# Kernel optimization log

Measured on AMD Instinct MI355X. Metric: run time of the kernel, lower is better.

The kernel has to match this reference:

```python
import jax, jax.numpy as jnp
import numpy as np

D_MODEL, D_INNER, D_STATE, HEADDIM, NHEADS, D_CONV, EPS = 2048, 4096, 64, 64, 64, 4, 1e-5
CONV_DIM = D_INNER + 2 * D_STATE  # ngroups=1


def setup_inputs() -> dict:
    key = jax.random.key(0)
    ks = jax.random.split(key, 8)
    return {
        "hidden_states": jax.random.normal(ks[0], (2, 2048, D_MODEL), jnp.float32),
        "rms_weight": jnp.ones((D_MODEL,), jnp.float32),
        "in_proj_w": jax.random.normal(ks[1], (2 * D_INNER + 2 * D_STATE + NHEADS, D_MODEL), jnp.float32) * 0.02,
        "conv_w": jax.random.normal(ks[2], (CONV_DIM, D_CONV), jnp.float32) * 0.2,
        "conv_b": jnp.zeros((CONV_DIM,), jnp.float32),
        "dt_bias": jax.random.normal(ks[3], (NHEADS,), jnp.float32) * 0.5,
        "A_log": jax.random.uniform(ks[4], (NHEADS,), jnp.float32, 0.0, 1.0),
        "D": jnp.ones((NHEADS,), jnp.float32),
        "norm_w": jnp.ones((D_INNER,), jnp.float32),
        "out_proj_w": jax.random.normal(ks[5], (D_MODEL, D_INNER), jnp.float32) * 0.02,
    }


def _rmsnorm(x, w, eps=EPS):
    var = jnp.mean(jnp.square(x), axis=-1, keepdims=True)
    return x * jax.lax.rsqrt(var + eps) * w


def reference(hidden_states, rms_weight, in_proj_w, conv_w, conv_b, dt_bias, A_log, D, norm_w, out_proj_w):
    b, l, _ = hidden_states.shape
    residual = hidden_states
    u = _rmsnorm(hidden_states, rms_weight)
    zxbcdt = jnp.einsum("bld,ed->ble", u, in_proj_w)
    z = zxbcdt[..., :D_INNER]
    xBC = zxbcdt[..., D_INNER:D_INNER + CONV_DIM]
    dt = zxbcdt[..., D_INNER + CONV_DIM:]  # (b, l, h)

    # causal depthwise conv1d over seq
    xBC_t = jnp.transpose(xBC, (0, 2, 1))  # (b, c, l)
    kernel = conv_w[:, None, :]  # (c, 1, k)
    xBC_t = jax.lax.conv_general_dilated(
        xBC_t, kernel, window_strides=(1,), padding=[(D_CONV - 1, 0)],
        feature_group_count=CONV_DIM,
        dimension_numbers=("NCH", "OIH", "NCH"))
    xBC = jax.nn.silu(jnp.transpose(xBC_t, (0, 2, 1)) + conv_b)

    x = xBC[..., :D_INNER].reshape(b, l, NHEADS, HEADDIM)
    B = xBC[..., D_INNER:D_INNER + D_STATE]  # (b, l, n)
    C = xBC[..., D_INNER + D_STATE:]         # (b, l, n)

    dt = jax.nn.softplus(dt + dt_bias)  # (b, l, h)
    A = -jnp.exp(A_log)                 # (h,)
    dA = jnp.exp(dt * A)                # (b, l, h)

    # sequential selective scan over time
    def step(state, inp):
        dA_t, dt_t, x_t, B_t, C_t = inp  # (b,h), (b,h), (b,h,p), (b,n), (b,n)
        state = state * dA_t[:, :, None, None] + jnp.einsum(
            "bh,bhp,bn->bhpn", dt_t, x_t, B_t)
        y_t = jnp.einsum("bhpn,bn->bhp", state, C_t)
        return state, y_t

    xs = (jnp.moveaxis(dA, 1, 0), jnp.moveaxis(dt, 1, 0),
          jnp.moveaxis(x, 1, 0), jnp.moveaxis(B, 1, 0), jnp.moveaxis(C, 1, 0))
    state0 = jnp.zeros((b, NHEADS, HEADDIM, D_STATE), hidden_states.dtype)
    _, ys = jax.lax.scan(step, state0, xs)
    y = jnp.moveaxis(ys, 0, 1)  # (b, l, h, p)
    y = y + D[None, None, :, None] * x
    y = y.reshape(b, l, D_INNER)

    # gated RMSNorm, then output projection
    y = _rmsnorm(y * jax.nn.silu(z), norm_w)
    out = jnp.einsum("ble,de->bld", y, out_proj_w)
    return residual + out
```

## Files before the change

### kernel.cpp

```cpp
#include <hip/hip_runtime.h>
#include <stdint.h>

#define DEV static __device__ __forceinline__

typedef __attribute__((ext_vector_type(8))) __bf16 bf16x8;
typedef __attribute__((ext_vector_type(4))) float f32x4;
typedef __attribute__((ext_vector_type(16))) float f32x16;

DEV float b2f(unsigned short u) {
    union { unsigned int i; float f; } v; v.i = ((unsigned int)u) << 16; return v.f;
}
DEV unsigned short f2b(float f) {
    unsigned int u = __builtin_bit_cast(unsigned int, f);
    unsigned int r = (u + 0x7FFFu + ((u >> 16) & 1u)) >> 16;
    return (unsigned short)r;
}
DEV f32x4 mfma16(bf16x8 a, bf16x8 b, f32x4 c) {
    return __builtin_amdgcn_mfma_f32_16x16x32_bf16(a, b, c, 0, 0, 0);
}
DEV f32x16 mfma32(bf16x8 a, bf16x8 b, f32x16 c) {
    return __builtin_amdgcn_mfma_f32_32x32x16_bf16(a, b, c, 0, 0, 0);
}

DEV void gload16(const void* g, void* l) {
    __builtin_amdgcn_global_load_lds(
        (const __attribute__((address_space(1))) void*)g,
        (__attribute__((address_space(3))) void*)l, 16, 0, 0);
}

__global__ __launch_bounds__(256) void k_cvt(
    const float* __restrict__ src, unsigned short* __restrict__ dst)
{
    long i = ((long)blockIdx.x * 256 + threadIdx.x) * 8;
    float4 a = *(const float4*)(src + i);
    float4 b = *(const float4*)(src + i + 4);
    union { uint4 v; unsigned short s[8]; } o;
    o.s[0] = f2b(a.x); o.s[1] = f2b(a.y); o.s[2] = f2b(a.z); o.s[3] = f2b(a.w);
    o.s[4] = f2b(b.x); o.s[5] = f2b(b.y); o.s[6] = f2b(b.z); o.s[7] = f2b(b.w);
    *(uint4*)(dst + i) = o.v;
}

__global__ __launch_bounds__(256) void k_rmsnorm_in(
    const float* __restrict__ h, const float* __restrict__ w,
    unsigned short* __restrict__ u)
{
    int row = blockIdx.x, t = threadIdx.x;
    const float* hp = h + (long)row * 2048 + t * 8;
    float4 a = *(const float4*)hp;
    float4 b = *(const float4*)(hp + 4);
    float x[8] = {a.x, a.y, a.z, a.w, b.x, b.y, b.z, b.w};
    float ss = 0.f;
#pragma unroll
    for (int i = 0; i < 8; i++) ss += x[i] * x[i];
#pragma unroll
    for (int o = 32; o > 0; o >>= 1) ss += __shfl_down(ss, o);
    __shared__ float red[4];
    if ((t & 63) == 0) red[t >> 6] = ss;
    __syncthreads();
    float tot = red[0] + red[1] + red[2] + red[3];
    float scale = rsqrtf(tot * (1.0f / 2048.0f) + 1e-5f);
    float4 wa = *(const float4*)(w + t * 8);
    float4 wb = *(const float4*)(w + t * 8 + 4);
    float wv[8] = {wa.x, wa.y, wa.z, wa.w, wb.x, wb.y, wb.z, wb.w};
    union { uint4 v; unsigned short s[8]; } ow;
#pragma unroll
    for (int i = 0; i < 8; i++) ow.s[i] = f2b(x[i] * scale * wv[i]);
    *(uint4*)(u + (long)row * 2048 + t * 8) = ow.v;
}

__global__ __launch_bounds__(512, 2) void k_gemm256(
    const unsigned short* __restrict__ A, const unsigned short* __restrict__ Bm,
    int K, unsigned short* __restrict__ Cb, int ldc)
{
    __shared__ __align__(16) char lds[131072];
    int tid = threadIdx.x;
    int w = tid >> 6, l = tid & 63;
    int NT = K >> 6, NI = K >> 7;
    long Kb = (long)K * 2;

    int nwg = gridDim.x * gridDim.y;
    int cpx = nwg >> 3;
    int fl = blockIdx.y * gridDim.x + blockIdx.x;
    int swz = (fl & 7) * cpx + (fl >> 3);
    long m0 = (long)(swz % gridDim.x) * 256;
    long n0 = (long)(swz / gridDim.x) * 256;

    int rl = tid >> 3;
    int csw16 = (((tid & 7) ^ (rl & 7)) << 4);
    const char* pA0 = (const char*)A + (m0 + rl) * Kb + csw16;
    const char* pA1 = (const char*)A + (m0 + 64 + rl) * Kb + csw16;
    const char* pB0 = (const char*)Bm + (n0 + rl) * Kb + csw16;
    const char* pB1 = (const char*)Bm + (n0 + 64 + rl) * Kb + csw16;
    int ldst = tid * 16;

#define STG(P0, P1, RGN, kt, half) do { if ((kt) < NT) {                      \
    char* Lr_ = lds + (((kt) & 1) << 16) + (RGN) + ((half) << 14);            \
    long go_ = (long)(half) * 128 * Kb + (long)(kt) * 128;                    \
    gload16((P0) + go_, Lr_ + ldst);                                          \
    gload16((P1) + go_, Lr_ + 8192 + ldst); } } while (0)

    int lq = l >> 4, lr15 = l & 15, key = l & 7;
    int off0 = ((lq ^ key) << 4);
    int off1 = (((4 + lq) ^ key) << 4);
    int aB = ((w >> 2) * 128 + lr15) * 128;
    int bB = 32768 + (((w & 3) * 64 + lr15) * 128);

    bf16x8 aF[4][2], b0F[2][2], b1F[2][2];
    f32x4 acc[8][4];
#pragma unroll
    for (int s = 0; s < 8; s++)
#pragma unroll
        for (int t = 0; t < 4; t++) acc[s][t] = (f32x4){0.f, 0.f, 0.f, 0.f};

#define DS_A(mh, BUF) do {                                                    \
    const char* ba_ = lds + (BUF) + aB + (mh) * 8192;                         \
    _Pragma("unroll") for (int s_ = 0; s_ < 4; s_++) {                        \
        aF[s_][0] = *(const bf16x8*)(ba_ + s_ * 2048 + off0);                 \
        aF[s_][1] = *(const bf16x8*)(ba_ + s_ * 2048 + off1); } } while (0)

#define DS_B(DST, nh, BUF) do {                                               \
    const char* bb_ = lds + (BUF) + bB + (nh) * 4096;                         \
    _Pragma("unroll") for (int t_ = 0; t_ < 2; t_++) {                        \
        DST[t_][0] = *(const bf16x8*)(bb_ + t_ * 2048 + off0);                \
        DST[t_][1] = *(const bf16x8*)(bb_ + t_ * 2048 + off1); } } while (0)

#define MQ(mh, nh, BF) do {                                                   \
    __builtin_amdgcn_s_setprio(1);                                            \
    _Pragma("unroll") for (int kk_ = 0; kk_ < 2; kk_++)                       \
    _Pragma("unroll") for (int s_ = 0; s_ < 4; s_++)                          \
    _Pragma("unroll") for (int t_ = 0; t_ < 2; t_++)                          \
        acc[(mh) * 4 + s_][(nh) * 2 + t_] =                                   \
            mfma16(aF[s_][kk_], BF[t_][kk_], acc[(mh) * 4 + s_][(nh) * 2 + t_]); \
    __builtin_amdgcn_s_setprio(0); } while (0)

#define BAR asm volatile("s_barrier" ::: "memory")
#define LGD asm volatile("s_waitcnt lgkmcnt(0)" ::: "memory")

    STG(pA0, pA1, 0,     0, 0);
    STG(pA0, pA1, 0,     0, 1);
    STG(pB0, pB1, 32768, 0, 0);
    STG(pB0, pB1, 32768, 0, 1);
    STG(pB0, pB1, 32768, 1, 0);
    STG(pB0, pB1, 32768, 1, 1);
    STG(pA0, pA1, 0,     1, 0);
    asm volatile("s_waitcnt vmcnt(6)" ::: "memory");
    BAR;

    for (int it = 0; it < NI; ++it) {
        int k1 = 2 * it + 1, k2 = 2 * it + 2, k3 = 2 * it + 3;
        DS_A(0, 0); DS_B(b0F, 0, 0);
        STG(pA0, pA1, 0, k1, 1);
        BAR; MQ(0, 0, b0F); LGD; BAR;
        DS_B(b1F, 1, 0);
        BAR; MQ(0, 1, b1F); LGD; BAR;
        DS_A(1, 0);
        STG(pB0, pB1, 32768, k2, 0);
        BAR; MQ(1, 1, b1F); LGD; BAR;
        STG(pB0, pB1, 32768, k2, 1);
        BAR; MQ(1, 0, b0F);
        if (it == NI - 1) { asm volatile("s_waitcnt vmcnt(0)" ::: "memory"); }
        else              { asm volatile("s_waitcnt vmcnt(4)" ::: "memory"); }
        BAR;
        DS_A(0, 65536); DS_B(b0F, 0, 65536);
        STG(pA0, pA1, 0, k2, 0);
        BAR; MQ(0, 0, b0F); LGD; BAR;
        DS_B(b1F, 1, 65536);
        STG(pA0, pA1, 0, k2, 1);
        BAR; MQ(0, 1, b1F); LGD; BAR;
        DS_A(1, 65536);
        STG(pB0, pB1, 32768, k3, 0);
        BAR; MQ(1, 1, b1F); LGD; BAR;
        STG(pB0, pB1, 32768, k3, 1);
        STG(pA0, pA1, 0, k3, 0);
        BAR; MQ(1, 0, b0F);
        if (it < NI - 1) { asm volatile("s_waitcnt vmcnt(6)" ::: "memory"); }
        BAR;
    }

    int colb = (w & 3) * 64 + lr15;
    int rowb = (w >> 2) * 128 + lq * 4;
#pragma unroll
    for (int s = 0; s < 8; s++)
#pragma unroll
        for (int t = 0; t < 4; t++) {
            long col = n0 + colb + t * 16;
            long row = m0 + rowb + s * 16;
#pragma unroll
            for (int r = 0; r < 4; r++)
                Cb[(row + r) * ldc + col] = f2b(acc[s][t][r]);
        }
#undef STG
#undef DS_A
#undef DS_B
#undef MQ
#undef BAR
#undef LGD
}

template <int EPI>
__global__ __launch_bounds__(256) void k_gemm_bt(
    const unsigned short* __restrict__ A, const unsigned short* __restrict__ Bm,
    int K, int nvalid, unsigned short* __restrict__ Cb, float* __restrict__ Cf,
    int ldc, const float* __restrict__ Res)
{
    __shared__ __align__(16) unsigned short sA[128 * 64];
    __shared__ __align__(16) unsigned short sB[128 * 64];
    int t = threadIdx.x;
    int w = t >> 6, L = t & 63;

    int flat = blockIdx.y * gridDim.x + blockIdx.x;
    int per = gridDim.x * 8;
    int strip = flat / per;
    int rem = flat - strip * per;
    long m0 = (long)(strip * 8 + (rem & 7)) * 128;
    long n0 = (long)(rem >> 3) * 128;

    int rloc = t >> 3;
    int c16  = t & 7;
    int csw  = c16 ^ (rloc & 7);
    const unsigned short* gAp[4];
    const unsigned short* gBp[4];
#pragma unroll
    for (int i = 0; i < 4; i++) {
        gAp[i] = A + (m0 + i * 32 + rloc) * (long)K + csw * 8;
        long rb = n0 + i * 32 + rloc;
        if (rb >= nvalid) rb = nvalid - 1;
        gBp[i] = Bm + rb * (long)K + csw * 8;
    }
    unsigned short* lA = sA + t * 8;
    unsigned short* lB = sB + t * 8;

    int mw = (w >> 1) * 64, nw = (w & 1) * 64;
    int rowA = mw + (L & 31), rowB = nw + (L & 31);
    int swA = (rowA & 7) << 4, swB = (rowB & 7) << 4;
    int q16 = (L >> 5) * 16;
    const char* pA = (const char*)sA + rowA * 128;
    const char* pB = (const char*)sB + rowB * 128;

    f32x16 acc[2][2];
#pragma unroll
    for (int ti = 0; ti < 2; ti++)
#pragma unroll
        for (int tj = 0; tj < 2; tj++)
#pragma unroll
            for (int r = 0; r < 16; r++) acc[ti][tj][r] = 0.f;

    for (int kt = 0; kt < K; kt += 64) {
#pragma unroll
        for (int i = 0; i < 4; i++) {
            gload16(gAp[i], lA + i * 2048);
            gload16(gBp[i], lB + i * 2048);
            gAp[i] += 64; gBp[i] += 64;
        }
        __syncthreads();
#pragma unroll
        for (int kk = 0; kk < 4; kk++) {
            bf16x8 af[2], bf[2];
#pragma unroll
            for (int ti = 0; ti < 2; ti++)
                af[ti] = *(const bf16x8*)(pA + ti * 4096 + ((q16 + kk * 32) ^ swA));
#pragma unroll
            for (int tj = 0; tj < 2; tj++)
                bf[tj] = *(const bf16x8*)(pB + tj * 4096 + ((q16 + kk * 32) ^ swB));
#pragma unroll
            for (int ti = 0; ti < 2; ti++)
#pragma unroll
                for (int tj = 0; tj < 2; tj++)
                    acc[ti][tj] = mfma32(af[ti], bf[tj], acc[ti][tj]);
        }
        __syncthreads();
    }
    int colL = L & 31;
    int rL = (L >> 5) * 4;
#pragma unroll
    for (int ti = 0; ti < 2; ti++)
#pragma unroll
        for (int tj = 0; tj < 2; tj++) {
            long c = n0 + nw + tj * 32 + colL;
            if (c >= nvalid) continue;
#pragma unroll
            for (int r = 0; r < 16; r++) {
                long row = m0 + mw + ti * 32 + (r & 3) + 8 * (r >> 2) + rL;
                float v = acc[ti][tj][r];
                if (EPI == 0) Cb[row * ldc + c] = f2b(v);
                else          Cf[row * ldc + c] = v + Res[row * ldc + c];
            }
        }
}

__global__ __launch_bounds__(128) void k_conv(
    const unsigned short* __restrict__ zx, const float* __restrict__ cw,
    const float* __restrict__ cb, unsigned short* __restrict__ xbc)
{
    int b = blockIdx.z;
    int l0 = blockIdx.y * 64;
    if (blockIdx.x < 4) {
        int c0 = blockIdx.x * 1024 + threadIdx.x * 8;
        float w0[8], w1[8], w2[8], w3[8], bias[8];
#pragma unroll
        for (int j = 0; j < 8; j++) {
            float4 wv = *(const float4*)(cw + (c0 + j) * 4);
            w0[j] = wv.x; w1[j] = wv.y; w2[j] = wv.z; w3[j] = wv.w;
            bias[j] = cb[c0 + j];
        }
        const unsigned short* src = zx + ((long)b * 2048) * 8384 + 4096 + c0;
        union { uint4 v; unsigned short s[8]; } h3, h2, h1;
        if (l0 >= 1) h1.v = *(const uint4*)(src + (long)(l0 - 1) * 8384);
        if (l0 >= 2) h2.v = *(const uint4*)(src + (long)(l0 - 2) * 8384);
        if (l0 >= 3) h3.v = *(const uint4*)(src + (long)(l0 - 3) * 8384);
        float xm3[8], xm2[8], xm1[8];
#pragma unroll
        for (int j = 0; j < 8; j++) {
            xm1[j] = (l0 >= 1) ? b2f(h1.s[j]) : 0.f;
            xm2[j] = (l0 >= 2) ? b2f(h2.s[j]) : 0.f;
            xm3[j] = (l0 >= 3) ? b2f(h3.s[j]) : 0.f;
        }
        const unsigned short* s2 = src + (long)l0 * 8384;
        unsigned short* dst = xbc + ((long)(b * 2048 + l0)) * 4224 + c0;
#pragma unroll 2
        for (int i = 0; i < 64; i++) {
            union { uint4 v; unsigned short s[8]; } xi, oo;
            xi.v = *(const uint4*)s2; s2 += 8384;
#pragma unroll
            for (int j = 0; j < 8; j++) {
                float xl = b2f(xi.s[j]);
                float a = xm3[j] * w0[j] + xm2[j] * w1[j] + xm1[j] * w2[j]
                        + xl * w3[j] + bias[j];
                a = a / (1.f + expf(-a));
                oo.s[j] = f2b(a);
                xm3[j] = xm2[j]; xm2[j] = xm1[j]; xm1[j] = xl;
            }
            *(uint4*)dst = oo.v; dst += 4224;
        }
    } else {
        int c = 4096 + threadIdx.x;
        float w0 = cw[c * 4 + 0], w1 = cw[c * 4 + 1];
        float w2 = cw[c * 4 + 2], w3 = cw[c * 4 + 3];
        float bias = cb[c];
        const unsigned short* src = zx + ((long)b * 2048) * 8384 + 4096 + c;
        float xm3 = (l0 >= 3) ? b2f(src[(long)(l0 - 3) * 8384]) : 0.f;
        float xm2 = (l0 >= 2) ? b2f(src[(long)(l0 - 2) * 8384]) : 0.f;
        float xm1 = (l0 >= 1) ? b2f(src[(long)(l0 - 1) * 8384]) : 0.f;
        const unsigned short* s2 = src + (long)l0 * 8384;
        unsigned short* dst = xbc + ((long)(b * 2048 + l0)) * 4224 + c;
#pragma unroll 8
        for (int i = 0; i < 64; i++) {
            float xl = b2f(*s2); s2 += 8384;
            float a = xm3 * w0 + xm2 * w1 + xm1 * w2 + xl * w3 + bias;
            a = a / (1.f + expf(-a));
            *dst = f2b(a); dst += 4224;
            xm3 = xm2; xm2 = xm1; xm1 = xl;
        }
    }
}

__global__ __launch_bounds__(256) void k_chunk_state_mfma(
    const unsigned short* __restrict__ xbc, const unsigned short* __restrict__ zxdt,
    const float* __restrict__ dt_bias, const float* __restrict__ A_log,
    unsigned short* __restrict__ Sbuf, float* __restrict__ dAtot)
{
    int blk = blockIdx.x;
    int c = blk & 7, bh = blk >> 3;
    int b = bh >> 6, h = bh & 63;
    int tid = threadIdx.x;
    int w = tid >> 6, L = tid & 63;
    int quad = L >> 4, col = L & 15;
    int rowBlk = (w >> 1) * 32, colBlk = (w & 1) * 32;
    __shared__ __align__(16) unsigned short sXp[64 * 72];
    __shared__ __align__(16) unsigned short sBn[64 * 72];
    __shared__ float sdt[64], sL[64];
    float Ah = expf(A_log[h]);
    float dtb = dt_bias[h];
    f32x4 acc[2][2];
#pragma unroll
    for (int ti = 0; ti < 2; ti++)
#pragma unroll
        for (int tj = 0; tj < 2; tj++) acc[ti][tj] = (f32x4){0.f, 0.f, 0.f, 0.f};
    float sumL = 0.f;

    for (int sub = 0; sub < 4; sub++) {
        int l0 = c * 256 + sub * 64;
        {
            int t = tid >> 2, pc = tid & 3;
            const unsigned short* gX = xbc + (long)(b * 2048 + l0 + t) * 4224 + h * 64 + pc * 16;
            union { uint4 v; unsigned short s[8]; } x0, x1;
            x0.v = *(const uint4*)gX; x1.v = *(const uint4*)(gX + 8);
#pragma unroll
            for (int j = 0; j < 8; j++) {
                sXp[(pc * 16 + j) * 72 + t] = x0.s[j];
                sXp[(pc * 16 + 8 + j) * 72 + t] = x1.s[j];
            }
        }
        if (tid < 64) {
            float raw = b2f(zxdt[((long)(b * 2048 + l0 + tid)) * 8384 + 8320 + h]) + dtb;
            float dtv = (raw > 20.f) ? raw : log1pf(expf(raw));
            float cum = dtv;
#pragma unroll
            for (int off = 1; off < 64; off <<= 1) {
                float v = __shfl_up(cum, off);
                if (tid >= off) cum += v;
            }
            sdt[tid] = dtv;
            sL[tid] = -Ah * cum;
        }
        __syncthreads();
        float Lend = sL[63];
        {
            int t = tid >> 2, nc = tid & 3;
            float wt = sdt[t] * __expf(Lend - sL[t]);
            const unsigned short* gB = xbc + (long)(b * 2048 + l0 + t) * 4224 + 4096 + nc * 16;
            union { uint4 v; unsigned short s[8]; } x0, x1;
            x0.v = *(const uint4*)gB; x1.v = *(const uint4*)(gB + 8);
#pragma unroll
            for (int j = 0; j < 8; j++) {
                sBn[(nc * 16 + j) * 72 + t] = f2b(b2f(x0.s[j]) * wt);
                sBn[(nc * 16 + 8 + j) * 72 + t] = f2b(b2f(x1.s[j]) * wt);
            }
        }
        __syncthreads();
        float e_end = __expf(Lend);
        sumL += Lend;
#pragma unroll
        for (int ti = 0; ti < 2; ti++)
#pragma unroll
            for (int tj = 0; tj < 2; tj++)
#pragma unroll
                for (int r = 0; r < 4; r++) acc[ti][tj][r] *= e_end;
#pragma unroll
        for (int kb = 0; kb < 2; kb++) {
            bf16x8 ax[2], bx[2];
#pragma unroll
            for (int ti = 0; ti < 2; ti++)
                ax[ti] = *(const bf16x8*)(sXp + (rowBlk + ti * 16 + col) * 72 + kb * 32 + quad * 8);
#pragma unroll
            for (int tj = 0; tj < 2; tj++)
                bx[tj] = *(const bf16x8*)(sBn + (colBlk + tj * 16 + col) * 72 + kb * 32 + quad * 8);
#pragma unroll
            for (int ti = 0; ti < 2; ti++)
#pragma unroll
                for (int tj = 0; tj < 2; tj++)
                    acc[ti][tj] = mfma16(ax[ti], bx[tj], acc[ti][tj]);
        }
        __syncthreads();
    }
#pragma unroll
    for (int ti = 0; ti < 2; ti++)
#pragma unroll
        for (int tj = 0; tj < 2; tj++)
#pragma unroll
            for (int r = 0; r < 4; r++) {
                int p = rowBlk + ti * 16 + quad * 4 + r;
                int n = colBlk + tj * 16 + col;
                Sbuf[(long)blk * 4096 + p * 64 + n] = f2b(acc[ti][tj][r]);
            }
    if (tid == 0) dAtot[blk] = __expf(sumL);
}

__global__ __launch_bounds__(256) void k_scan_chunk_mfma(
    const unsigned short* __restrict__ xbc, const unsigned short* __restrict__ zxdt,
    const float* __restrict__ dt_bias, const float* __restrict__ A_log,
    const float* __restrict__ Dv,
    const unsigned short* __restrict__ Sbuf, const float* __restrict__ dAtot,
    unsigned short* __restrict__ yout)
{
    int blk = blockIdx.x;
    int c = blk & 7, bh = blk >> 3;
    int b = bh >> 6, h = bh & 63;
    int tid = threadIdx.x;
    int w = tid >> 6, L = tid & 63;
    int quad = L >> 4, col = L & 15;
    int rowBlk = (w >> 1) * 32, colBlk = (w & 1) * 32;
    __shared__ __align__(16) unsigned short sCm[64 * 72];
    __shared__ __align__(16) unsigned short sBtMs[64 * 72];
    __shared__ __align__(16) unsigned short sXp[64 * 72];
    __shared__ __align__(16) unsigned short sBn[64 * 72];
    __shared__ __align__(16) unsigned short sHb[64 * 72];
    __shared__ float sdt[64], sL[64], sEs[64];
    float Ah = expf(A_log[h]);
    float dtb = dt_bias[h];
    float Dh = Dv[h];

    f32x4 acc_h[2][2];
#pragma unroll
    for (int ti = 0; ti < 2; ti++)
#pragma unroll
        for (int tj = 0; tj < 2; tj++) acc_h[ti][tj] = (f32x4){0.f, 0.f, 0.f, 0.f};
    int sb = bh * 8;
    for (int j = 0; j < c; j++) {
        float d = dAtot[sb + j];
        const unsigned short* Sp = Sbuf + (long)(sb + j) * 4096;
#pragma unroll
        for (int ti = 0; ti < 2; ti++)
#pragma unroll
            for (int tj = 0; tj < 2; tj++)
#pragma unroll
                for (int r = 0; r < 4; r++) {
                    int p = rowBlk + ti * 16 + quad * 4 + r;
                    int n = colBlk + tj * 16 + col;
                    acc_h[ti][tj][r] = acc_h[ti][tj][r] * d + b2f(Sp[p * 64 + n]);
                }
    }

    for (int sub = 0; sub < 4; sub++) {
        int l0 = c * 256 + sub * 64;
        {
            int row = tid >> 2, c4 = tid & 3;
            const unsigned short* gR = xbc + (long)(b * 2048 + l0 + row) * 4224;
            uint4 v0 = *(const uint4*)(gR + 4160 + c4 * 8);
            uint4 v1 = *(const uint4*)(gR + 4160 + (c4 + 4) * 8);
            *(uint4*)(sCm + row * 72 + c4 * 8) = v0;
            *(uint4*)(sCm + row * 72 + (c4 + 4) * 8) = v1;
            uint4 w0 = *(const uint4*)(gR + 4096 + c4 * 8);
            uint4 w1 = *(const uint4*)(gR + 4096 + (c4 + 4) * 8);
            *(uint4*)(sBtMs + row * 72 + c4 * 8) = w0;
            *(uint4*)(sBtMs + row * 72 + (c4 + 4) * 8) = w1;
        }
        {
            int t = tid >> 2, pc = tid & 3;
            const unsigned short* gX = xbc + (long)(b * 2048 + l0 + t) * 4224 + h * 64 + pc * 16;
            union { uint4 v; unsigned short s[8]; } x0, x1;
            x0.v = *(const uint4*)gX; x1.v = *(const uint4*)(gX + 8);
#pragma unroll
            for (int j = 0; j < 8; j++) {
                sXp[(pc * 16 + j) * 72 + t] = x0.s[j];
                sXp[(pc * 16 + 8 + j) * 72 + t] = x1.s[j];
            }
        }
        if (tid < 64) {
            float raw = b2f(zxdt[((long)(b * 2048 + l0 + tid)) * 8384 + 8320 + h]) + dtb;
            float dtv = (raw > 20.f) ? raw : log1pf(expf(raw));
            float cum = dtv;
#pragma unroll
            for (int off = 1; off < 64; off <<= 1) {
                float v = __shfl_up(cum, off);
                if (tid >= off) cum += v;
            }
            sdt[tid] = dtv;
            float l = -Ah * cum;
            sL[tid] = l;
            sEs[tid] = __expf(l);
        }
        __syncthreads();
        float Lend = sL[63];
        {
            int t = tid >> 2, nc = tid & 3;
            float wt = sdt[t] * __expf(Lend - sL[t]);
            const unsigned short* gB = xbc + (long)(b * 2048 + l0 + t) * 4224 + 4096 + nc * 16;
            union { uint4 v; unsigned short s[8]; } x0, x1;
            x0.v = *(const uint4*)gB; x1.v = *(const uint4*)(gB + 8);
#pragma unroll
            for (int j = 0; j < 8; j++) {
                sBn[(nc * 16 + j) * 72 + t] = f2b(b2f(x0.s[j]) * wt);
                sBn[(nc * 16 + 8 + j) * 72 + t] = f2b(b2f(x1.s[j]) * wt);
            }
        }
#pragma unroll
        for (int ti = 0; ti < 2; ti++)
#pragma unroll
            for (int tj = 0; tj < 2; tj++)
#pragma unroll
                for (int r = 0; r < 4; r++) {
                    int p = rowBlk + ti * 16 + quad * 4 + r;
                    int n = colBlk + tj * 16 + col;
                    sHb[p * 72 + n] = f2b(acc_h[ti][tj][r]);
                }
        __syncthreads();
        f32x4 g[2][2];
#pragma unroll
        for (int ti = 0; ti < 2; ti++)
#pragma unroll
            for (int tj = 0; tj < 2; tj++) g[ti][tj] = (f32x4){0.f, 0.f, 0.f, 0.f};
#pragma unroll
        for (int kb = 0; kb < 2; kb++) {
            bf16x8 ac[2], bc[2];
#pragma unroll
            for (int ti = 0; ti < 2; ti++)
                ac[ti] = *(const bf16x8*)(sCm + (rowBlk + ti * 16 + col) * 72 + kb * 32 + quad * 8);
#pragma unroll
            for (int tj = 0; tj < 2; tj++)
                bc[tj] = *(const bf16x8*)(sBtMs + (colBlk + tj * 16 + col) * 72 + kb * 32 + quad * 8);
#pragma unroll
            for (int ti = 0; ti < 2; ti++)
#pragma unroll
                for (int tj = 0; tj < 2; tj++)
                    g[ti][tj] = mfma16(ac[ti], bc[tj], g[ti][tj]);
        }
        __syncthreads();
#pragma unroll
        for (int tj = 0; tj < 2; tj++) {
            int t_idx = colBlk + tj * 16 + col;
            float lt = sL[t_idx], dtt = sdt[t_idx];
#pragma unroll
            for (int ti = 0; ti < 2; ti++)
#pragma unroll
                for (int r = 0; r < 4; r++) {
                    int s_idx = rowBlk + ti * 16 + quad * 4 + r;
                    float m = (t_idx <= s_idx) ? g[ti][tj][r] * dtt * __expf(sL[s_idx] - lt) : 0.f;
                    sBtMs[s_idx * 72 + t_idx] = f2b(m);
                }
        }
        __syncthreads();
        f32x4 yv[2][2];
#pragma unroll
        for (int ti = 0; ti < 2; ti++)
#pragma unroll
            for (int tj = 0; tj < 2; tj++) yv[ti][tj] = (f32x4){0.f, 0.f, 0.f, 0.f};
#pragma unroll
        for (int kb = 0; kb < 2; kb++) {
            bf16x8 am[2], bxp[2];
#pragma unroll
            for (int ti = 0; ti < 2; ti++)
                am[ti] = *(const bf16x8*)(sBtMs + (rowBlk + ti * 16 + col) * 72 + kb * 32 + quad * 8);
#pragma unroll
            for (int tj = 0; tj < 2; tj++)
                bxp[tj] = *(const bf16x8*)(sXp + (colBlk + tj * 16 + col) * 72 + kb * 32 + quad * 8);
#pragma unroll
            for (int ti = 0; ti < 2; ti++)
#pragma unroll
                for (int tj = 0; tj < 2; tj++)
                    yv[ti][tj] = mfma16(am[ti], bxp[tj], yv[ti][tj]);
        }
        float es0 = sEs[rowBlk + col], es1 = sEs[rowBlk + 16 + col];
#pragma unroll
        for (int kb = 0; kb < 2; kb++) {
            bf16x8 acx[2], bhh[2];
#pragma unroll
            for (int ti = 0; ti < 2; ti++) {
                union { bf16x8 v; unsigned short s[8]; } a;
                a.v = *(const bf16x8*)(sCm + (rowBlk + ti * 16 + col) * 72 + kb * 32 + quad * 8);
                float es = ti ? es1 : es0;
#pragma unroll
                for (int j = 0; j < 8; j++) a.s[j] = f2b(b2f(a.s[j]) * es);
                acx[ti] = a.v;
            }
#pragma unroll
            for (int tj = 0; tj < 2; tj++)
                bhh[tj] = *(const bf16x8*)(sHb + (colBlk + tj * 16 + col) * 72 + kb * 32 + quad * 8);
#pragma unroll
            for (int ti = 0; ti < 2; ti++)
#pragma unroll
                for (int tj = 0; tj < 2; tj++)
                    yv[ti][tj] = mfma16(acx[ti], bhh[tj], yv[ti][tj]);
        }
        float e_end = __expf(Lend);
#pragma unroll
        for (int ti = 0; ti < 2; ti++)
#pragma unroll
            for (int tj = 0; tj < 2; tj++)
#pragma unroll
                for (int r = 0; r < 4; r++) acc_h[ti][tj][r] *= e_end;
#pragma unroll
        for (int kb = 0; kb < 2; kb++) {
            bf16x8 ax[2], bn[2];
#pragma unroll
            for (int ti = 0; ti < 2; ti++)
                ax[ti] = *(const bf16x8*)(sXp + (rowBlk + ti * 16 + col) * 72 + kb * 32 + quad * 8);
#pragma unroll
            for (int tj = 0; tj < 2; tj++)
                bn[tj] = *(const bf16x8*)(sBn + (colBlk + tj * 16 + col) * 72 + kb * 32 + quad * 8);
#pragma unroll
            for (int ti = 0; ti < 2; ti++)
#pragma unroll
                for (int tj = 0; tj < 2; tj++)
                    acc_h[ti][tj] = mfma16(ax[ti], bn[tj], acc_h[ti][tj]);
        }
#pragma unroll
        for (int ti = 0; ti < 2; ti++)
#pragma unroll
            for (int tj = 0; tj < 2; tj++)
#pragma unroll
                for (int r = 0; r < 4; r++) {
                    int s_idx = rowBlk + ti * 16 + quad * 4 + r;
                    int p = colBlk + tj * 16 + col;
                    float xv = b2f(sXp[p * 72 + s_idx]);
                    float yo = yv[ti][tj][r] + Dh * xv;
                    yout[((long)(b * 2048 + l0 + s_idx)) * 8384 + 4096 + h * 64 + p] = f2b(yo);
                }
        __syncthreads();
    }
}

__global__ __launch_bounds__(256) void k_gatenorm(
    const unsigned short* __restrict__ zx, const float* __restrict__ nw,
    unsigned short* __restrict__ y2)
{
    int row = blockIdx.x, t = threadIdx.x;
    const unsigned short* zr = zx + (long)row * 8384;
    union { uint4 v; unsigned short s[8]; } za, zb, ya, yb;
    za.v = *(const uint4*)(zr + t * 16);
    zb.v = *(const uint4*)(zr + t * 16 + 8);
    ya.v = *(const uint4*)(zr + 4096 + t * 16);
    yb.v = *(const uint4*)(zr + 4096 + t * 16 + 8);
    float v[16]; float ss = 0.f;
#pragma unroll
    for (int i = 0; i < 8; i++) {
        float z = b2f(za.s[i]);
        float g = b2f(ya.s[i]) * (z / (1.f + expf(-z)));
        v[i] = g; ss += g * g;
    }
#pragma unroll
    for (int i = 0; i < 8; i++) {
        float z = b2f(zb.s[i]);
        float g = b2f(yb.s[i]) * (z / (1.f + expf(-z)));
        v[8 + i] = g; ss += g * g;
    }
#pragma unroll
    for (int o = 32; o > 0; o >>= 1) ss += __shfl_down(ss, o);
    __shared__ float red[4];
    if ((t & 63) == 0) red[t >> 6] = ss;
    __syncthreads();
    float tot = red[0] + red[1] + red[2] + red[3];
    float scale = rsqrtf(tot * (1.0f / 4096.0f) + 1e-5f);
    float4 n0 = *(const float4*)(nw + t * 16);
    float4 n1 = *(const float4*)(nw + t * 16 + 4);
    float4 n2 = *(const float4*)(nw + t * 16 + 8);
    float4 n3 = *(const float4*)(nw + t * 16 + 12);
    float nv[16] = {n0.x, n0.y, n0.z, n0.w, n1.x, n1.y, n1.z, n1.w,
                    n2.x, n2.y, n2.z, n2.w, n3.x, n3.y, n3.z, n3.w};
    union { uint4 u4; unsigned short s[8]; } o0, o1;
#pragma unroll
    for (int i = 0; i < 8; i++) o0.s[i] = f2b(v[i] * scale * nv[i]);
#pragma unroll
    for (int i = 0; i < 8; i++) o1.s[i] = f2b(v[8 + i] * scale * nv[8 + i]);
    unsigned short* yo = y2 + (long)row * 4096 + t * 16;
    *(uint4*)yo = o0.u4;
    *(uint4*)(yo + 8) = o1.u4;
}

extern "C" void kernel_launch(void* const* d_in, const int* in_sizes, int n_in,
                              void* d_out, int out_size, void* d_ws, size_t ws_size,
                              hipStream_t stream)
{
    const float* h    = (const float*)d_in[0];
    const float* rmsw = (const float*)d_in[1];
    const float* w1   = (const float*)d_in[2];
    const float* cw   = (const float*)d_in[3];
    const float* cbp  = (const float*)d_in[4];
    const float* dtb  = (const float*)d_in[5];
    const float* alog = (const float*)d_in[6];
    const float* Dv   = (const float*)d_in[7];
    const float* nw   = (const float*)d_in[8];
    const float* w2   = (const float*)d_in[9];

    char* ws = (char*)d_ws;
    unsigned short* zx    = (unsigned short*)ws;
    unsigned short* w1b   = (unsigned short*)(ws + 68681728L);
    unsigned short* xbc   = (unsigned short*)(ws + 68681728L);
    unsigned short* y2    = (unsigned short*)(ws + 68681728L);
    unsigned short* u     = (unsigned short*)(ws + 103284736L);
    unsigned short* Sbuf  = (unsigned short*)(ws + 103284736L);
    float*          dAt   = (float*)(ws + 111673344L);
    unsigned short* w2b   = (unsigned short*)(ws + 103284736L);
    float* outp = (float*)d_out;

    k_rmsnorm_in<<<4096, 256, 0, stream>>>(h, rmsw, u);
    k_cvt<<<8384, 256, 0, stream>>>(w1, w1b);
    k_gemm256<<<dim3(16, 32), 512, 0, stream>>>(u, w1b, 2048, zx, 8384);
    k_gemm_bt<0><<<dim3(2, 32), 256, 0, stream>>>(
        u, w1b + 8192L * 2048, 2048, 192, zx + 8192, nullptr, 8384, nullptr);
    k_conv<<<dim3(5, 32, 2), 128, 0, stream>>>(zx, cw, cbp, xbc);
    k_chunk_state_mfma<<<1024, 256, 0, stream>>>(xbc, zx, dtb, alog, Sbuf, dAt);
    k_scan_chunk_mfma<<<1024, 256, 0, stream>>>(xbc, zx, dtb, alog, Dv, Sbuf, dAt, zx);
    k_gatenorm<<<4096, 256, 0, stream>>>(zx, nw, y2);
    k_cvt<<<4096, 256, 0, stream>>>(w2, w2b);
    k_gemm_bt<1><<<dim3(16, 32), 256, 0, stream>>>(y2, w2b, 4096, 2048, nullptr, outp, 2048, h);
}
```

Before: 563.0 us.

## Use 256x128-tile triple-buffered GEMM kernel for output projection

Replaces the 128x128-tile 256-thread GEMM for the output projection with a new 512-thread kernel that computes 256x128 tiles. It uses a three-stage LDS ring with XOR-swizzled layout, split M-halves interleaved with global prefetch, and an XCD-aware block swizzle. The residual add is fused into the epilogue. The aim is more data reuse per tile and better overlap of loads with MFMA work. The trade-off is half as many workgroups (256) and one workgroup per CU because of the large LDS footprint.

New measurement: 558.5 us. Within noise of the previous version (-0.8%).

```diff
diff --git a/kernel.cpp b/kernel.cpp
--- a/kernel.cpp
+++ b/kernel.cpp
@@ -197,6 +197,119 @@
 #undef LGD
 }
 
+__global__ __launch_bounds__(512, 1) void k_gemm2(
+    const unsigned short* __restrict__ A, const unsigned short* __restrict__ Bm,
+    int K, float* __restrict__ Cf, int ldc, const float* __restrict__ Res)
+{
+    __shared__ __align__(16) char lds[147456];
+    int tid = threadIdx.x;
+    int w = tid >> 6, l = tid & 63;
+    int NT = K >> 6;
+    long Kb = (long)K * 2;
+
+    int nwg = gridDim.x * gridDim.y;
+    int cpx = nwg >> 3;
+    int fl = blockIdx.y * gridDim.x + blockIdx.x;
+    int swz = (fl & 7) * cpx + (fl >> 3);
+    long m0 = (long)(swz % gridDim.x) * 256;
+    long n0 = (long)(swz / gridDim.x) * 128;
+
+    int rl = tid >> 3;
+    int csw16 = (((tid & 7) ^ (rl & 7)) << 4);
+    const char* pA0 = (const char*)A + (m0 + rl) * Kb + csw16;
+    const char* pA1 = (const char*)A + (m0 + 64 + rl) * Kb + csw16;
+    const char* pB0 = (const char*)Bm + (n0 + rl) * Kb + csw16;
+    int ldst = tid * 16;
+
+#define STG_A(kt) do { if ((kt) < NT) {                                       \
+    char* L_ = lds + ((kt) % 3) * 49152;                                      \
+    long g0_ = (long)(kt) * 128;                                              \
+    gload16(pA0 + g0_, L_ + ldst);                                            \
+    gload16(pA1 + g0_, L_ + 8192 + ldst);                                     \
+    gload16(pA0 + 128 * Kb + g0_, L_ + 16384 + ldst);                         \
+    gload16(pA1 + 128 * Kb + g0_, L_ + 24576 + ldst); } } while (0)
+#define STG_B(kt) do { if ((kt) < NT) {                                       \
+    char* L_ = lds + ((kt) % 3) * 49152 + 32768;                              \
+    long g0_ = (long)(kt) * 128;                                              \
+    gload16(pB0 + g0_, L_ + ldst);                                            \
+    gload16(pB0 + 64 * Kb + g0_, L_ + 8192 + ldst); } } while (0)
+
+    int lq = l >> 4, lr15 = l & 15, key = l & 7;
+    int off0 = ((lq ^ key) << 4);
+    int off1 = (((4 + lq) ^ key) << 4);
+    int aB = ((w >> 2) * 128 + lr15) * 128;
+    int bB = 32768 + (((w & 3) * 32 + lr15) * 128);
+
+    bf16x8 aF[4][2], bF[2][2];
+    f32x4 acc[8][2];
+#pragma unroll
+    for (int s = 0; s < 8; s++)
+#pragma unroll
+        for (int t = 0; t < 2; t++) acc[s][t] = (f32x4){0.f, 0.f, 0.f, 0.f};
+
+#define DS_A2(mh, BUF) do {                                                   \
+    const char* ba_ = lds + (BUF) + aB + (mh) * 8192;                         \
+    _Pragma("unroll") for (int s_ = 0; s_ < 4; s_++) {                        \
+        aF[s_][0] = *(const bf16x8*)(ba_ + s_ * 2048 + off0);                 \
+        aF[s_][1] = *(const bf16x8*)(ba_ + s_ * 2048 + off1); } } while (0)
+
+#define DS_B2(BUF) do {                                                       \
+    const char* bb_ = lds + (BUF) + bB;                                       \
+    _Pragma("unroll") for (int t_ = 0; t_ < 2; t_++) {                        \
+        bF[t_][0] = *(const bf16x8*)(bb_ + t_ * 2048 + off0);                 \
+        bF[t_][1] = *(const bf16x8*)(bb_ + t_ * 2048 + off1); } } while (0)
+
+#define MQ2(mh) do {                                                          \
+    __builtin_amdgcn_s_setprio(1);                                            \
+    _Pragma("unroll") for (int kk_ = 0; kk_ < 2; kk_++)                       \
+    _Pragma("unroll") for (int s_ = 0; s_ < 4; s_++)                          \
+    _Pragma("unroll") for (int t_ = 0; t_ < 2; t_++)                          \
+        acc[(mh) * 4 + s_][t_] =                                              \
+            mfma16(aF[s_][kk_], bF[t_][kk_], acc[(mh) * 4 + s_][t_]);         \
+    __builtin_amdgcn_s_setprio(0); } while (0)
+
+#define BAR asm volatile("s_barrier" ::: "memory")
+#define LGD asm volatile("s_waitcnt lgkmcnt(0)" ::: "memory")
+
+    STG_B(0); STG_A(0); STG_B(1); STG_A(1);
+    asm volatile("s_waitcnt vmcnt(6)" ::: "memory");
+    BAR;
+
+    for (int kt = 0; kt < NT; ++kt) {
+        int buf = (kt % 3) * 49152;
+        DS_A2(0, buf); DS_B2(buf);
+        STG_B(kt + 2);
+        BAR; MQ2(0); LGD; BAR;
+        DS_A2(1, buf);
+        STG_A(kt + 2);
+        BAR; MQ2(1); LGD;
+        if (kt < NT - 2)       { asm volatile("s_waitcnt vmcnt(6)" ::: "memory"); }
+        else if (kt == NT - 2) { asm volatile("s_waitcnt vmcnt(0)" ::: "memory"); }
+        BAR;
+    }
+
+    long colb = n0 + (w & 3) * 32 + lr15;
+    long rowb = m0 + (w >> 2) * 128 + lq * 4;
+#pragma unroll
+    for (int s = 0; s < 8; s++)
+#pragma unroll
+        for (int t = 0; t < 2; t++) {
+            long col = colb + t * 16;
+#pragma unroll
+            for (int r = 0; r < 4; r++) {
+                long row = rowb + s * 16 + r;
+                Cf[row * ldc + col] = acc[s][t][r] + Res[row * ldc + col];
+            }
+        }
+#undef STG_A
+#undef STG_B
+#undef DS_A2
+#undef DS_B2
+#undef MQ2
+#undef BAR
+#undef LGD
+}
+
 template <int EPI>
 __global__ __launch_bounds__(256) void k_gemm_bt(
     const unsigned short* __restrict__ A, const unsigned short* __restrict__ Bm,
@@ -763,5 +876,5 @@
     k_scan_chunk_mfma<<<1024, 256, 0, stream>>>(xbc, zx, dtb, alog, Dv, Sbuf, dAt, zx);
     k_gatenorm<<<4096, 256, 0, stream>>>(zx, nw, y2);
     k_cvt<<<4096, 256, 0, stream>>>(w2, w2b);
-    k_gemm_bt<1><<<dim3(16, 32), 256, 0, stream>>>(y2, w2b, 4096, 2048, nullptr, outp, 2048, h);
-}
+    k_gemm2<<<dim3(16, 16), 512, 0, stream>>>(y2, w2b, 4096, outp, 2048, h);
+}
```
